# Optimization experiments

Measured on AMD Instinct MI355X. Metric: run time of the kernel, lower is better.

Reference implementation:

```python
import jax, jax.numpy as jnp
import numpy as np

NUM_HEADS = 8
CODEBOOK_SIZE = 1024
HEAD_DIM = 128
BATCH = 32768


def setup_inputs() -> dict:
    key = jax.random.key(0)
    k_z, k_cb = jax.random.split(key)
    z = jax.random.normal(k_z, (BATCH, NUM_HEADS * HEAD_DIM), dtype=jnp.float32)
    codebooks = jax.random.normal(k_cb, (NUM_HEADS, CODEBOOK_SIZE, HEAD_DIM), dtype=jnp.float32)
    return {"z": z, "codebooks": codebooks}


def reference(z, codebooks):
    # z: [B, H*D]; codebooks: [H, K, D]
    H, K, D = codebooks.shape
    B = z.shape[0]
    zh = z.reshape(B, H, D)
    # Squared euclidean distances ||z - c||^2 = ||z||^2 - 2 z.c + ||c||^2.
    # torch.cdist(p=2) applies sqrt, but sqrt is monotone so argmin is identical.
    z_sq = jnp.sum(zh * zh, axis=-1)                       # [B, H]
    c_sq = jnp.sum(codebooks * codebooks, axis=-1)         # [H, K]
    cross = jnp.einsum('bhd,hkd->bhk', zh, codebooks)      # [B, H, K]
    d2 = z_sq[:, :, None] - 2.0 * cross + c_sq[None, :, :]  # [B, H, K]
    idx = jnp.argmin(d2, axis=-1)                          # [B, H] int
    # Gather nearest codes per head: codebooks[h, idx[b,h]] -> [B, H, D]
    zq = codebooks[jnp.arange(H)[None, :], idx]
    # Straight-through estimator: forward = codes, backward = identity on z.
    zq = zh + jax.lax.stop_gradient(zq - zh)
    return zq.reshape(B, H * D), idx
```

## Files before the change

kernel.cpp:

```cpp
#include <hip/hip_runtime.h>

namespace {
constexpr int kNH = 8;
constexpr int kK  = 1024;
constexpr int kD  = 128;
constexpr int kB  = 32768;

constexpr int BM  = 128;
constexpr int kMarginQ = 4;
constexpr float kMarginF32 = 0.0625f;

constexpr size_t kOffCsq  = 4096;
constexpr size_t kOffCbF  = 65536;
constexpr size_t kOffPart = 65536 + 4194304;
constexpr size_t kOffWl6  = 65536 + 8388608;
constexpr size_t kOffWl5  = 65536 + 4194304;
}

typedef short           bf16x8 __attribute__((ext_vector_type(8)));
typedef unsigned short  us16x8 __attribute__((ext_vector_type(8)));
typedef float           f32x16 __attribute__((ext_vector_type(16)));

__device__ __forceinline__ unsigned short f2bf_rne(float f) {
    unsigned int x = __float_as_uint(f);
    unsigned int r = (x + 0x7fffu + ((x >> 16) & 1u)) >> 16;
    return (unsigned short)r;
}
__device__ __forceinline__ float bf2f(unsigned short u) {
    return __uint_as_float(((unsigned int)u) << 16);
}
__device__ __forceinline__ int med3_i32(int a, int b, int c) {
    int d;
    asm("v_med3_i32 %0, %1, %2, %3" : "=v"(d) : "v"(a), "v"(b), "v"(c));
    return d;
}

__global__ void pq_prep(const float* __restrict__ cb,
                        unsigned short* __restrict__ cbf,
                        float* __restrict__ csq)
{
    int code = blockIdx.x;
    int t = threadIdx.x;
    int h = code >> 10, k = code & 1023;
    int kt = k >> 6, cv = (k >> 5) & 1, l31 = k & 31;
    int kc = t >> 4, hh = (t >> 3) & 1, j = t & 7;
    float v = cb[(size_t)code * kD + t];
    float vs = v * -2048.0f;
    unsigned short hb = f2bf_rne(vs);
    unsigned short lb = f2bf_rne(vs - bf2f(hb));
    size_t base = ((((size_t)h * 16 + kt) * 8 + kc) * 2 + cv) * 2048;
    size_t off  = base + (hh * 32 + l31) * 16 + j * 2;
    *(unsigned short*)((char*)cbf + off)        = hb;
    *(unsigned short*)((char*)cbf + off + 1024) = lb;
    __shared__ double red[128];
    red[t] = (double)v * (double)v;
    __syncthreads();
    for (int s = 64; s > 0; s >>= 1) {
        if (t < s) red[t] += red[t + s];
        __syncthreads();
    }
    if (t == 0) csq[code] = (float)(red[0] * 1024.0);
}

__global__ __launch_bounds__(512)
void pq_coarse_mfma7(const float* __restrict__ z,
                     const unsigned short* __restrict__ cbf,
                     const float* __restrict__ csq1024,
                     int2* __restrict__ part)
{
    __shared__ unsigned short zbuf[2][2][32 * kD];
    __shared__ int2  P[2][8][32];
    __shared__ float csel_s[8][2][2][16];

    const int t    = threadIdx.x;
    const int lane = t & 63;
    const int w    = t >> 6;
    const int l31  = lane & 31, h32 = lane >> 5;
    const int h    = blockIdx.y;
    const int half = blockIdx.z;
    const int rb0  = blockIdx.x * 1024;

    {
        int ww = t >> 6, hb2 = (t >> 5) & 1, idx = t & 31;
        int cv = idx >> 4, r = idx & 15;
        int cr = (r & 3) + ((r >> 2) << 3);
        csel_s[ww][hb2][cv][r] =
            csq1024[h * kK + half * 512 + ww * 64 + hb2 * 4 + cv * 32 + cr];
    }

    const int cgb = half * 512 + w * 64 + h32 * 4;
    int addv[2][16];
    #pragma unroll
    for (int cv = 0; cv < 2; ++cv)
        #pragma unroll
        for (int r = 0; r < 16; ++r)
            addv[cv][r] = cgb + cv * 32 + (r & 3) + ((r >> 2) << 3);

    bf16x8 Ah[8][2], Al[8][2];
    {
        const char* base = (const char*)cbf
            + (((size_t)h * 16 + half * 8 + w) * 16) * 2048 + lane * 16;
        #pragma unroll
        for (int kc = 0; kc < 8; ++kc)
            #pragma unroll
            for (int cv = 0; cv < 2; ++cv) {
                const char* p = base + (size_t)(kc * 2 + cv) * 2048;
                Ah[kc][cv] = *(const bf16x8*)p;
                Al[kc][cv] = *(const bf16x8*)(p + 1024);
            }
    }

    float4 zA, zB;
    auto issueZ = [&](int tile) {
        const float* zp = z + (size_t)(rb0 + tile * 32 + (t >> 4)) * (kNH * kD)
                            + h * kD + (t & 15) * 8;
        zA = *(const float4*)zp;
        zB = *(const float4*)(zp + 4);
    };
    auto commitZ = [&](int buf) {
        unsigned u0 = __float_as_uint(zA.x) + 0x8000u;
        unsigned u1 = __float_as_uint(zA.y) + 0x8000u;
        unsigned u2 = __float_as_uint(zA.z) + 0x8000u;
        unsigned u3 = __float_as_uint(zA.w) + 0x8000u;
        unsigned u4 = __float_as_uint(zB.x) + 0x8000u;
        unsigned u5 = __float_as_uint(zB.y) + 0x8000u;
        unsigned u6 = __float_as_uint(zB.z) + 0x8000u;
        unsigned u7 = __float_as_uint(zB.w) + 0x8000u;
        unsigned h01 = __builtin_amdgcn_perm(u1, u0, 0x07060302u);
        unsigned h23 = __builtin_amdgcn_perm(u3, u2, 0x07060302u);
        unsigned h45 = __builtin_amdgcn_perm(u5, u4, 0x07060302u);
        unsigned h67 = __builtin_amdgcn_perm(u7, u6, 0x07060302u);
        float r0 = zA.x - __uint_as_float(u0 & 0xffff0000u);
        float r1 = zA.y - __uint_as_float(u1 & 0xffff0000u);
        float r2 = zA.z - __uint_as_float(u2 & 0xffff0000u);
        float r3 = zA.w - __uint_as_float(u3 & 0xffff0000u);
        float r4 = zB.x - __uint_as_float(u4 & 0xffff0000u);
        float r5 = zB.y - __uint_as_float(u5 & 0xffff0000u);
        float r6 = zB.z - __uint_as_float(u6 & 0xffff0000u);
        float r7 = zB.w - __uint_as_float(u7 & 0xffff0000u);
        unsigned l01 = __builtin_amdgcn_perm(__float_as_uint(r1) + 0x8000u,
                                             __float_as_uint(r0) + 0x8000u, 0x07060302u);
        unsigned l23 = __builtin_amdgcn_perm(__float_as_uint(r3) + 0x8000u,
                                             __float_as_uint(r2) + 0x8000u, 0x07060302u);
        unsigned l45 = __builtin_amdgcn_perm(__float_as_uint(r5) + 0x8000u,
                                             __float_as_uint(r4) + 0x8000u, 0x07060302u);
        unsigned l67 = __builtin_amdgcn_perm(__float_as_uint(r7) + 0x8000u,
                                             __float_as_uint(r6) + 0x8000u, 0x07060302u);
        int rr = t >> 4, seg = t & 15;
        int off = rr * 256 + ((seg * 16) ^ ((rr & 15) << 4));
        uint4 hv = {h01, h23, h45, h67};
        uint4 lv = {l01, l23, l45, l67};
        *(uint4*)((char*)&zbuf[buf][0][0] + off) = hv;
        *(uint4*)((char*)&zbuf[buf][1][0] + off) = lv;
    };
    auto mergeP = [&](int pb, int tile) {
        int2 m = P[pb][0][t];
        int m1 = m.x, m2 = m.y;
        #pragma unroll
        for (int ww = 1; ww < 8; ++ww) {
            int2 p = P[pb][ww][t];
            int mx = max(m1, p.x);
            m1 = min(m1, p.x);
            m2 = min(min(m2, p.y), mx);
        }
        int gid = (rb0 + tile * 32 + t) * kNH + h;
        part[(size_t)gid * 2 + half] = make_int2(m1, m2);
    };

    issueZ(0);
    commitZ(0);
    __syncthreads();

    int cur = 0;
    for (int tile = 0; tile < 32; ++tile) {
        if (tile + 1 < 32) issueZ(tile + 1);
        if (tile > 0 && t < 32) mergeP(cur ^ 1, tile - 1);

        f32x16 acc0, acc1;
        __builtin_memcpy(&acc0, &csel_s[w][h32][0][0], 64);
        __builtin_memcpy(&acc1, &csel_s[w][h32][1][0], 64);

        const char* zh0 = (const char*)&zbuf[cur][0][0];
        const char* zl0 = (const char*)&zbuf[cur][1][0];
        const int boff = l31 * 256;
        const int swz  = (l31 & 15) << 4;
        __builtin_amdgcn_s_setprio(1);
        #pragma unroll
        for (int kc = 0; kc < 8; ++kc) {
            int col = (kc * 32 + h32 * 16) ^ swz;
            bf16x8 Bh = *(const bf16x8*)(zh0 + boff + col);
            bf16x8 Bl = *(const bf16x8*)(zl0 + boff + col);
            acc0 = __builtin_amdgcn_mfma_f32_32x32x16_bf16(Ah[kc][0], Bh, acc0, 0, 0, 0);
            acc1 = __builtin_amdgcn_mfma_f32_32x32x16_bf16(Ah[kc][1], Bh, acc1, 0, 0, 0);
            acc0 = __builtin_amdgcn_mfma_f32_32x32x16_bf16(Al[kc][0], Bh, acc0, 0, 0, 0);
            acc1 = __builtin_amdgcn_mfma_f32_32x32x16_bf16(Al[kc][1], Bh, acc1, 0, 0, 0);
            acc0 = __builtin_amdgcn_mfma_f32_32x32x16_bf16(Ah[kc][0], Bl, acc0, 0, 0, 0);
            acc1 = __builtin_amdgcn_mfma_f32_32x32x16_bf16(Ah[kc][1], Bl, acc1, 0, 0, 0);
        }
        __builtin_amdgcn_s_setprio(0);

        if (tile + 1 < 32) commitZ(cur ^ 1);

        int b1 = 0x7fffffff, b2 = 0x7fffffff;
        #pragma unroll
        for (int r = 0; r < 16; ++r) {
            {
                int key = (((int)acc0[r]) << 10) + addv[0][r];
                b2 = med3_i32(key, b1, b2);
                b1 = min(b1, key);
            }
            {
                int key = (((int)acc1[r]) << 10) + addv[1][r];
                b2 = med3_i32(key, b1, b2);
                b1 = min(b1, key);
            }
        }
        int o1 = __shfl_xor(b1, 32), o2 = __shfl_xor(b2, 32);
        int mx2 = max(b1, o1);
        int v1 = min(b1, o1);
        int v2 = min(min(b2, o2), mx2);
        if (h32 == 0) P[cur][w][l31] = make_int2(v1, v2);

        __syncthreads();
        cur ^= 1;
    }
    if (t < 32) mergeP(cur ^ 1, 31);
}

__global__ __launch_bounds__(256)
void pq_merge(const int2* __restrict__ part, const float* __restrict__ cb,
              float* __restrict__ out_zq, float* __restrict__ out_idx,
              unsigned int* wl_count, unsigned int* wl, unsigned int wl_cap)
{
    __shared__ int idx_s[128];
    const int t = threadIdx.x;
    const int g0 = blockIdx.x * 128;
    if (t < 128) {
        int gid = g0 + t;
        int2 p0 = part[(size_t)gid * 2];
        int2 p1 = part[(size_t)gid * 2 + 1];
        int mx = max(p0.x, p1.x);
        int v1 = min(p0.x, p1.x);
        int v2 = min(min(p0.y, p1.y), mx);
        int idx = v1 & 1023;
        idx_s[t] = idx;
        out_idx[gid] = (float)idx;
        if (wl_cap > 0u && ((v2 >> 10) - (v1 >> 10)) <= kMarginQ) {
            unsigned int pos = atomicAdd(wl_count, 1u);
            if (pos < wl_cap) wl[pos] = (unsigned int)gid;
        }
    }
    __syncthreads();
    #pragma unroll
    for (int it = 0; it < 16; ++it) {
        int c = it * 256 + t;
        int row = c >> 5, c4 = c & 31;
        int gid = g0 + row;
        int b = gid >> 3, hh = gid & 7;
        *(float4*)(out_zq + (size_t)b * (kNH * kD) + hh * kD + c4 * 4) =
            *(const float4*)(cb + ((size_t)hh * kK + idx_s[row]) * kD + c4 * 4);
    }
}

__global__ __launch_bounds__(256, 2)
void pq_coarse_mfma3(const float* __restrict__ z, const float* __restrict__ cb,
                     const unsigned short* __restrict__ cbf,
                     const float* __restrict__ csq1024,
                     float* __restrict__ out_zq, float* __restrict__ out_idx,
                     unsigned int* wl_count, unsigned int* wl, unsigned int wl_cap)
{
    __shared__ float csq_s[kK];
    __shared__ int   idx_s[BM];

    const int t    = threadIdx.x;
    const int h    = blockIdx.y;
    const int b0   = blockIdx.x * BM;
    const int lane = t & 63;
    const int w    = t >> 6;
    const int l31  = lane & 31, h32 = lane >> 5;

    *(float4*)&csq_s[t * 4] = *(const float4*)(csq1024 + h * kK + t * 4);

    bf16x8 Ah[8], Al[8];
    {
        const float* zr = z + (size_t)(b0 + w * 32 + l31) * (kNH * kD) + h * kD + h32 * 8;
        #pragma unroll
        for (int kc = 0; kc < 8; ++kc) {
            float4 a = *(const float4*)(zr + kc * 16);
            float4 b = *(const float4*)(zr + kc * 16 + 4);
            float f[8] = {a.x, a.y, a.z, a.w, b.x, b.y, b.z, b.w};
            bf16x8 hv, lv;
            #pragma unroll
            for (int j = 0; j < 8; ++j) {
                unsigned short hb = f2bf_rne(f[j]);
                hv[j] = (short)hb;
                lv[j] = (short)f2bf_rne(f[j] - bf2f(hb));
            }
            Ah[kc] = hv;
            Al[kc] = lv;
        }
    }
    __syncthreads();

    int b1[16], b2[16];
    #pragma unroll
    for (int r = 0; r < 16; ++r) { b1[r] = 0x7fffffff; b2[r] = 0x7fffffff; }

    const char* bbase = (const char*)cbf + (size_t)h * 524288 + lane * 16;
#define LDSLOT(kt_, kc_, s_)                                                  \
    {                                                                         \
        const char* p_ = bbase + (size_t)(((kt_) * 8 + (kc_)) * 2) * 2048;    \
        Bh0[s_] = *(const bf16x8*)(p_);                                       \
        Bl0[s_] = *(const bf16x8*)(p_ + 1024);                                \
        Bh1[s_] = *(const bf16x8*)(p_ + 2048);                                \
        Bl1[s_] = *(const bf16x8*)(p_ + 3072);                                \
    }

    bf16x8 Bh0[4], Bl0[4], Bh1[4], Bl1[4];
    LDSLOT(0, 0, 0);
    LDSLOT(0, 1, 1);

    for (int kt = 0; kt < 16; ++kt) {
        f32x16 acc0 = (f32x16)0.0f, acc1 = (f32x16)0.0f;
        const int ktn = (kt + 1 < 16) ? kt + 1 : kt;
        #pragma unroll
        for (int kc = 0; kc < 8; ++kc) {
            const int s  = kc & 3;
            const int s2 = (kc + 2) & 3;
            if (kc < 6) { LDSLOT(kt, kc + 2, s2); } else { LDSLOT(ktn, kc - 6, s2); }
            __builtin_amdgcn_s_setprio(1);
            acc0 = __builtin_amdgcn_mfma_f32_32x32x16_bf16(Ah[kc], Bh0[s], acc0, 0, 0, 0);
            acc1 = __builtin_amdgcn_mfma_f32_32x32x16_bf16(Ah[kc], Bh1[s], acc1, 0, 0, 0);
            acc0 = __builtin_amdgcn_mfma_f32_32x32x16_bf16(Al[kc], Bh0[s], acc0, 0, 0, 0);
            acc1 = __builtin_amdgcn_mfma_f32_32x32x16_bf16(Al[kc], Bh1[s], acc1, 0, 0, 0);
            acc0 = __builtin_amdgcn_mfma_f32_32x32x16_bf16(Ah[kc], Bl0[s], acc0, 0, 0, 0);
            acc1 = __builtin_amdgcn_mfma_f32_32x32x16_bf16(Ah[kc], Bl1[s], acc1, 0, 0, 0);
            __builtin_amdgcn_s_setprio(0);
        }
        const float cs0 = csq_s[kt * 64 + l31];
        const float cs1 = csq_s[kt * 64 + 32 + l31];
        const int   kg0 = kt * 64 + l31, kg1 = kg0 + 32;
        #pragma unroll
        for (int r = 0; r < 16; ++r) {
            {
                float kf = acc0[r] + cs0;
                int key = ((int)kf << 10) + kg0;
                int mx = max(b1[r], key); b1[r] = min(b1[r], key); b2[r] = min(b2[r], mx);
            }
            {
                float kf = acc1[r] + cs1;
                int key = ((int)kf << 10) + kg1;
                int mx = max(b1[r], key); b1[r] = min(b1[r], key); b2[r] = min(b2[r], mx);
            }
        }
    }
#undef LDSLOT

    #pragma unroll
    for (int r = 0; r < 16; ++r) {
        int v1 = b1[r], v2 = b2[r];
        #pragma unroll
        for (int m = 1; m < 32; m <<= 1) {
            int o1 = __shfl_xor(v1, m);
            int o2 = __shfl_xor(v2, m);
            int mx = max(v1, o1);
            v1 = min(v1, o1);
            v2 = min(min(v2, o2), mx);
        }
        if (l31 == 0) {
            int row = w * 32 + (r & 3) + ((r >> 2) << 3) + h32 * 4;
            int idx = v1 & 1023;
            idx_s[row] = idx;
            int gid = (b0 + row) * kNH + h;
            out_idx[gid] = (float)idx;
            if (wl_cap > 0u && ((v2 >> 10) - (v1 >> 10)) <= kMarginQ) {
                unsigned int pos = atomicAdd(wl_count, 1u);
                if (pos < wl_cap) wl[pos] = (unsigned int)gid;
            }
        }
    }
    __syncthreads();
    {
        const float* cbh_row = cb + (size_t)h * kK * kD;
        #pragma unroll
        for (int it = 0; it < 16; ++it) {
            int c = it * 256 + t;
            int row = c >> 5, col4 = c & 31;
            *(float4*)(out_zq + (size_t)(b0 + row) * (kNH * kD) + h * kD + col4 * 4) =
                *(const float4*)(cbh_row + (size_t)idx_s[row] * kD + col4 * 4);
        }
    }
}

__global__ __launch_bounds__(256, 2)
void pq_coarse_f32(const float* __restrict__ z, const float* __restrict__ cb,
                   float* __restrict__ out_zq, float* __restrict__ out_idx,
                   unsigned int* wl_count, unsigned int* wl, unsigned int wl_cap)
{
    constexpr int KT = 64, PAD = 68, BMF = 64;
    __shared__ float zT[kD][PAD];
    __shared__ float cT[kD][PAD];
    __shared__ float csq_s[KT];
    __shared__ int   bidx_s[BMF];

    const int t  = threadIdx.x;
    const int h  = blockIdx.y;
    const int b0 = blockIdx.x * BMF;
    const int tx = t & 15, ty = t >> 4;
    const int r8 = t & 7,  d4 = t >> 3;

    {
        const float* zp = z + (size_t)(b0 + r8) * (kNH * kD) + h * kD + 4 * d4;
        #pragma unroll
        for (int it = 0; it < BMF / 8; ++it) {
            float4 v = *(const float4*)(zp + (size_t)(8 * it) * (kNH * kD));
            int r = r8 + 8 * it;
            zT[4 * d4 + 0][r] = v.x; zT[4 * d4 + 1][r] = v.y;
            zT[4 * d4 + 2][r] = v.z; zT[4 * d4 + 3][r] = v.w;
        }
    }
    float best1[4], best2[4]; int ibest[4];
    #pragma unroll
    for (int i = 0; i < 4; ++i) { best1[i] = 3.4e38f; best2[i] = 3.4e38f; ibest[i] = 0; }

    for (int kt = 0; kt < kK / KT; ++kt) {
        __syncthreads();
        {
            const float* cp = cb + ((size_t)h * kK + kt * KT + r8) * kD + 4 * d4;
            #pragma unroll
            for (int it = 0; it < KT / 8; ++it) {
                float4 v = *(const float4*)(cp + (size_t)(8 * it) * kD);
                int r = r8 + 8 * it;
                cT[4 * d4 + 0][r] = v.x; cT[4 * d4 + 1][r] = v.y;
                cT[4 * d4 + 2][r] = v.z; cT[4 * d4 + 3][r] = v.w;
            }
        }
        if (t < KT) csq_s[t] = 0.0f;
        __syncthreads();
        {
            int kk = t & 63, part = t >> 6;
            float s = 0.f;
            #pragma unroll
            for (int i = 0; i < 32; ++i) { float v = cT[32 * part + i][kk]; s = fmaf(v, v, s); }
            atomicAdd(&csq_s[kk], s);
        }
        __syncthreads();
        float accA[4][4] = {{0}}, accB[4][4] = {{0}};
        #pragma unroll 2
        for (int d = 0; d < kD; d += 2) {
            float4 za = *(const float4*)&zT[d][4 * ty];
            float4 ca = *(const float4*)&cT[d][4 * tx];
            float4 zb = *(const float4*)&zT[d + 1][4 * ty];
            float4 cv = *(const float4*)&cT[d + 1][4 * tx];
            float zav[4] = {za.x, za.y, za.z, za.w}, cav[4] = {ca.x, ca.y, ca.z, ca.w};
            float zbv[4] = {zb.x, zb.y, zb.z, zb.w}, cbv[4] = {cv.x, cv.y, cv.z, cv.w};
            #pragma unroll
            for (int i = 0; i < 4; ++i)
                #pragma unroll
                for (int j = 0; j < 4; ++j) {
                    accA[i][j] = fmaf(zav[i], cav[j], accA[i][j]);
                    accB[i][j] = fmaf(zbv[i], cbv[j], accB[i][j]);
                }
        }
        #pragma unroll
        for (int j = 0; j < 4; ++j) {
            int kk = 4 * tx + j;
            float cs = csq_s[kk];
            int kg = kt * KT + kk;
            #pragma unroll
            for (int i = 0; i < 4; ++i) {
                float s = fmaf(-2.0f, accA[i][j] + accB[i][j], cs);
                if (s < best1[i]) { best2[i] = best1[i]; best1[i] = s; ibest[i] = kg; }
                else if (s < best2[i]) { best2[i] = s; }
            }
        }
    }
    __syncthreads();
    float* redv1 = &zT[0][0];
    float* redv2 = redv1 + BMF * 16;
    int*   redi  = (int*)(redv2 + BMF * 16);
    #pragma unroll
    for (int i = 0; i < 4; ++i) {
        int r = 4 * ty + i;
        redv1[r * 16 + tx] = best1[i]; redv2[r * 16 + tx] = best2[i]; redi[r * 16 + tx] = ibest[i];
    }
    __syncthreads();
    if (t < BMF) {
        int r = t;
        float vb1_ = redv1[r * 16], vb2_ = redv2[r * 16];
        int i1 = redi[r * 16];
        #pragma unroll
        for (int x = 1; x < 16; ++x) {
            float nb1 = redv1[r * 16 + x], nb2 = redv2[r * 16 + x];
            int ni1 = redi[r * 16 + x];
            if (nb1 < vb1_ || (nb1 == vb1_ && ni1 < i1)) { vb2_ = fminf(vb1_, nb2); vb1_ = nb1; i1 = ni1; }
            else vb2_ = fminf(vb2_, nb1);
        }
        bidx_s[r] = i1;
        int gid = (b0 + r) * kNH + h;
        out_idx[gid] = (float)i1;
        if (wl_cap > 0u && (vb2_ - vb1_) <= kMarginF32) {
            unsigned int pos = atomicAdd(wl_count, 1u);
            if (pos < wl_cap) wl[pos] = (unsigned int)gid;
        }
    }
    __syncthreads();
    {
        int r = t >> 2, q = t & 3;
        const float* src = cb + ((size_t)h * kK + bidx_s[r]) * kD;
        float* dst = out_zq + (size_t)(b0 + r) * (kNH * kD) + h * kD;
        #pragma unroll
        for (int m = 0; m < 8; ++m) {
            int jj = 4 * m + q;
            *(float4*)(dst + 4 * jj) = *(const float4*)(src + 4 * jj);
        }
    }
}

__global__ __launch_bounds__(256)
void pq_exact(const float* __restrict__ z, const float* __restrict__ cb,
              float* __restrict__ out_zq, float* __restrict__ out_idx,
              const unsigned int* wl_count, const unsigned int* wl,
              unsigned int wl_cap)
{
    if (wl_cap == 0u) return;
    __shared__ float  zs[kD];
    __shared__ double rv[256];
    __shared__ int    ri[256];
    unsigned int n = *wl_count;
    if (n > wl_cap) n = wl_cap;
    const int t = threadIdx.x;
    for (unsigned int e = blockIdx.x; e < n; e += gridDim.x) {
        unsigned int id = wl[e];
        int b = (int)(id / kNH), h = (int)(id % kNH);
        if (t < kD) zs[t] = z[(size_t)b * (kNH * kD) + h * kD + t];
        __syncthreads();
        double bv = 1e300; int bi = 0;
        #pragma unroll
        for (int kk = 0; kk < 4; ++kk) {
            int k = t * 4 + kk;
            const float* c = cb + ((size_t)h * kK + k) * kD;
            double s = 0.0;
            for (int d = 0; d < kD; ++d) {
                double diff = (double)zs[d] - (double)c[d];
                s = fma(diff, diff, s);
            }
            if (s < bv) { bv = s; bi = k; }
        }
        rv[t] = bv; ri[t] = bi;
        __syncthreads();
        for (int s2 = 128; s2 > 0; s2 >>= 1) {
            if (t < s2) {
                if (rv[t + s2] < rv[t] || (rv[t + s2] == rv[t] && ri[t + s2] < ri[t])) {
                    rv[t] = rv[t + s2]; ri[t] = ri[t + s2];
                }
            }
            __syncthreads();
        }
        int kbest = ri[0];
        if (t == 0) out_idx[id] = (float)kbest;
        if (t < kD)
            out_zq[(size_t)b * (kNH * kD) + h * kD + t] =
                cb[((size_t)h * kK + kbest) * kD + t];
        __syncthreads();
    }
}

extern "C" void kernel_launch(void* const* d_in, const int* in_sizes, int n_in,
                              void* d_out, int out_size, void* d_ws, size_t ws_size,
                              hipStream_t stream)
{
    const float* z  = (const float*)d_in[0];
    const float* cb = (const float*)d_in[1];
    float* out_zq  = (float*)d_out;
    float* out_idx = out_zq + (size_t)kB * kNH * kD;
    char* ws = (char*)d_ws;

    if (ws_size >= kOffWl6 + 65536) {
        unsigned int* wl_count = (unsigned int*)ws;
        unsigned int* wl = (unsigned int*)(ws + kOffWl6);
        size_t c = (ws_size - kOffWl6) / 4;
        unsigned int cap = (unsigned int)(c > 262144 ? 262144 : c);
        float* csq = (float*)(ws + kOffCsq);
        unsigned short* cbf = (unsigned short*)(ws + kOffCbF);
        int2* part = (int2*)(ws + kOffPart);

        hipMemsetAsync(d_ws, 0, 4, stream);
        pq_prep<<<kNH * kK, kD, 0, stream>>>(cb, cbf, csq);
        dim3 grid(32, kNH, 2);
        pq_coarse_mfma7<<<grid, 512, 0, stream>>>(z, cbf, csq, part);
        pq_merge<<<kB * kNH / 128, 256, 0, stream>>>(part, cb, out_zq, out_idx,
                                                     wl_count, wl, cap);
        pq_exact<<<256, 256, 0, stream>>>(z, cb, out_zq, out_idx, wl_count, wl, cap);
    } else if (ws_size >= kOffWl5 + 4096) {
        unsigned int* wl_count = (unsigned int*)ws;
        unsigned int* wl = (unsigned int*)(ws + kOffWl5);
        size_t c = (ws_size - kOffWl5) / 4;
        unsigned int cap = (unsigned int)(c > 262144 ? 262144 : c);
        float* csq = (float*)(ws + kOffCsq);
        unsigned short* cbf = (unsigned short*)(ws + kOffCbF);

        hipMemsetAsync(d_ws, 0, 4, stream);
        pq_prep<<<kNH * kK, kD, 0, stream>>>(cb, cbf, csq);
        dim3 grid(kB / BM, kNH);
        pq_coarse_mfma3<<<grid, 256, 0, stream>>>(z, cb, cbf, csq,
                                                  out_zq, out_idx, wl_count, wl, cap);
        pq_exact<<<256, 256, 0, stream>>>(z, cb, out_zq, out_idx, wl_count, wl, cap);
    } else {
        unsigned int* wl_count = (unsigned int*)ws;
        unsigned int* wl = wl_count + 1;
        unsigned int cap = 0;
        if (ws_size >= 64) {
            size_t c = ws_size / 4 - 1;
            cap = (unsigned int)(c > 262144 ? 262144 : c);
            hipMemsetAsync(d_ws, 0, 4, stream);
        }
        dim3 grid(kB / 64, kNH);
        pq_coarse_f32<<<grid, 256, 0, stream>>>(z, cb, out_zq, out_idx, wl_count, wl, cap);
        pq_exact<<<256, 256, 0, stream>>>(z, cb, out_zq, out_idx, wl_count, wl, cap);
    }
}
```

Baseline: 226.4 us.

## Cover full codebook per block with 1024 threads, drop two-half partial merge

The coarse MFMA kernel now uses 16 waves per block so one block scans all 1024 codes for its rows instead of splitting the codebook into two halves across blocks. This halves redundant z loads and conversion, halves the partial-result buffer, and removes the two-way merge in pq_merge. In exchange the grid has half as many blocks, each with 1024 threads, which may lower occupancy and latency hiding and lengthens the intra-block merge.

```diff
diff --git a/kernel.cpp b/kernel.cpp
--- a/kernel.cpp
+++ b/kernel.cpp
@@ -13,12 +13,11 @@
 constexpr size_t kOffCsq  = 4096;
 constexpr size_t kOffCbF  = 65536;
 constexpr size_t kOffPart = 65536 + 4194304;
-constexpr size_t kOffWl6  = 65536 + 8388608;
+constexpr size_t kOffWl10 = 65536 + 4194304 + 2097152;
 constexpr size_t kOffWl5  = 65536 + 4194304;
 }
 
 typedef short           bf16x8 __attribute__((ext_vector_type(8)));
-typedef unsigned short  us16x8 __attribute__((ext_vector_type(8)));
 typedef float           f32x16 __attribute__((ext_vector_type(16)));
 
 __device__ __forceinline__ unsigned short f2bf_rne(float f) {
@@ -62,22 +61,21 @@
     if (t == 0) csq[code] = (float)(red[0] * 1024.0);
 }
 
-__global__ __launch_bounds__(512)
-void pq_coarse_mfma7(const float* __restrict__ z,
-                     const unsigned short* __restrict__ cbf,
-                     const float* __restrict__ csq1024,
-                     int2* __restrict__ part)
+__global__ __launch_bounds__(1024)
+void pq_coarse_mfma10(const float* __restrict__ z,
+                      const unsigned short* __restrict__ cbf,
+                      const float* __restrict__ csq1024,
+                      int2* __restrict__ part)
 {
     __shared__ unsigned short zbuf[2][2][32 * kD];
-    __shared__ int2  P[2][8][32];
-    __shared__ float csel_s[8][2][2][16];
+    __shared__ int2  P[2][16][32];
+    __shared__ float csel_s[16][2][2][16];
 
     const int t    = threadIdx.x;
     const int lane = t & 63;
     const int w    = t >> 6;
     const int l31  = lane & 31, h32 = lane >> 5;
     const int h    = blockIdx.y;
-    const int half = blockIdx.z;
     const int rb0  = blockIdx.x * 1024;
 
     {
@@ -85,10 +83,10 @@
         int cv = idx >> 4, r = idx & 15;
         int cr = (r & 3) + ((r >> 2) << 3);
         csel_s[ww][hb2][cv][r] =
-            csq1024[h * kK + half * 512 + ww * 64 + hb2 * 4 + cv * 32 + cr];
-    }
-
-    const int cgb = half * 512 + w * 64 + h32 * 4;
+            csq1024[h * kK + ww * 64 + hb2 * 4 + cv * 32 + cr];
+    }
+
+    const int cgb = w * 64 + h32 * 4;
     int addv[2][16];
     #pragma unroll
     for (int cv = 0; cv < 2; ++cv)
@@ -99,7 +97,7 @@
     bf16x8 Ah[8][2], Al[8][2];
     {
         const char* base = (const char*)cbf
-            + (((size_t)h * 16 + half * 8 + w) * 16) * 2048 + lane * 16;
+            + (((size_t)h * 16 + w) * 16) * 2048 + lane * 16;
         #pragma unroll
         for (int kc = 0; kc < 8; ++kc)
             #pragma unroll
@@ -110,61 +108,44 @@
             }
     }
 
-    float4 zA, zB;
+    float4 zA;
     auto issueZ = [&](int tile) {
-        const float* zp = z + (size_t)(rb0 + tile * 32 + (t >> 4)) * (kNH * kD)
-                            + h * kD + (t & 15) * 8;
-        zA = *(const float4*)zp;
-        zB = *(const float4*)(zp + 4);
+        zA = *(const float4*)(z + (size_t)(rb0 + tile * 32 + (t >> 5)) * (kNH * kD)
+                                + h * kD + (t & 31) * 4);
     };
     auto commitZ = [&](int buf) {
         unsigned u0 = __float_as_uint(zA.x) + 0x8000u;
         unsigned u1 = __float_as_uint(zA.y) + 0x8000u;
         unsigned u2 = __float_as_uint(zA.z) + 0x8000u;
         unsigned u3 = __float_as_uint(zA.w) + 0x8000u;
-        unsigned u4 = __float_as_uint(zB.x) + 0x8000u;
-        unsigned u5 = __float_as_uint(zB.y) + 0x8000u;
-        unsigned u6 = __float_as_uint(zB.z) + 0x8000u;
-        unsigned u7 = __float_as_uint(zB.w) + 0x8000u;
         unsigned h01 = __builtin_amdgcn_perm(u1, u0, 0x07060302u);
         unsigned h23 = __builtin_amdgcn_perm(u3, u2, 0x07060302u);
-        unsigned h45 = __builtin_amdgcn_perm(u5, u4, 0x07060302u);
-        unsigned h67 = __builtin_amdgcn_perm(u7, u6, 0x07060302u);
         float r0 = zA.x - __uint_as_float(u0 & 0xffff0000u);
         float r1 = zA.y - __uint_as_float(u1 & 0xffff0000u);
         float r2 = zA.z - __uint_as_float(u2 & 0xffff0000u);
         float r3 = zA.w - __uint_as_float(u3 & 0xffff0000u);
-        float r4 = zB.x - __uint_as_float(u4 & 0xffff0000u);
-        float r5 = zB.y - __uint_as_float(u5 & 0xffff0000u);
-        float r6 = zB.z - __uint_as_float(u6 & 0xffff0000u);
-        float r7 = zB.w - __uint_as_float(u7 & 0xffff0000u);
         unsigned l01 = __builtin_amdgcn_perm(__float_as_uint(r1) + 0x8000u,
                                              __float_as_uint(r0) + 0x8000u, 0x07060302u);
         unsigned l23 = __builtin_amdgcn_perm(__float_as_uint(r3) + 0x8000u,
                                              __float_as_uint(r2) + 0x8000u, 0x07060302u);
-        unsigned l45 = __builtin_amdgcn_perm(__float_as_uint(r5) + 0x8000u,
-                                             __float_as_uint(r4) + 0x8000u, 0x07060302u);
-        unsigned l67 = __builtin_amdgcn_perm(__float_as_uint(r7) + 0x8000u,
-                                             __float_as_uint(r6) + 0x8000u, 0x07060302u);
-        int rr = t >> 4, seg = t & 15;
-        int off = rr * 256 + ((seg * 16) ^ ((rr & 15) << 4));
-        uint4 hv = {h01, h23, h45, h67};
-        uint4 lv = {l01, l23, l45, l67};
-        *(uint4*)((char*)&zbuf[buf][0][0] + off) = hv;
-        *(uint4*)((char*)&zbuf[buf][1][0] + off) = lv;
+        int rr = t >> 5, c4 = t & 31;
+        int off = rr * 256 + ((((c4 >> 1) * 16)) ^ ((rr & 15) << 4)) + (c4 & 1) * 8;
+        uint2 hv = {h01, h23};
+        uint2 lv = {l01, l23};
+        *(uint2*)((char*)&zbuf[buf][0][0] + off) = hv;
+        *(uint2*)((char*)&zbuf[buf][1][0] + off) = lv;
     };
     auto mergeP = [&](int pb, int tile) {
         int2 m = P[pb][0][t];
         int m1 = m.x, m2 = m.y;
         #pragma unroll
-        for (int ww = 1; ww < 8; ++ww) {
+        for (int ww = 1; ww < 16; ++ww) {
             int2 p = P[pb][ww][t];
             int mx = max(m1, p.x);
             m1 = min(m1, p.x);
             m2 = min(min(m2, p.y), mx);
         }
-        int gid = (rb0 + tile * 32 + t) * kNH + h;
-        part[(size_t)gid * 2 + half] = make_int2(m1, m2);
+        part[(size_t)(rb0 + tile * 32 + t) * kNH + h] = make_int2(m1, m2);
     };
 
     issueZ(0);
@@ -237,15 +218,11 @@
     const int g0 = blockIdx.x * 128;
     if (t < 128) {
         int gid = g0 + t;
-        int2 p0 = part[(size_t)gid * 2];
-        int2 p1 = part[(size_t)gid * 2 + 1];
-        int mx = max(p0.x, p1.x);
-        int v1 = min(p0.x, p1.x);
-        int v2 = min(min(p0.y, p1.y), mx);
-        int idx = v1 & 1023;
+        int2 p = part[gid];
+        int idx = p.x & 1023;
         idx_s[t] = idx;
         out_idx[gid] = (float)idx;
-        if (wl_cap > 0u && ((v2 >> 10) - (v1 >> 10)) <= kMarginQ) {
+        if (wl_cap > 0u && ((p.y >> 10) - (p.x >> 10)) <= kMarginQ) {
             unsigned int pos = atomicAdd(wl_count, 1u);
             if (pos < wl_cap) wl[pos] = (unsigned int)gid;
         }
@@ -576,10 +553,10 @@
     float* out_idx = out_zq + (size_t)kB * kNH * kD;
     char* ws = (char*)d_ws;
 
-    if (ws_size >= kOffWl6 + 65536) {
+    if (ws_size >= kOffWl10 + 65536) {
         unsigned int* wl_count = (unsigned int*)ws;
-        unsigned int* wl = (unsigned int*)(ws + kOffWl6);
-        size_t c = (ws_size - kOffWl6) / 4;
+        unsigned int* wl = (unsigned int*)(ws + kOffWl10);
+        size_t c = (ws_size - kOffWl10) / 4;
         unsigned int cap = (unsigned int)(c > 262144 ? 262144 : c);
         float* csq = (float*)(ws + kOffCsq);
         unsigned short* cbf = (unsigned short*)(ws + kOffCbF);
@@ -587,8 +564,8 @@
 
         hipMemsetAsync(d_ws, 0, 4, stream);
         pq_prep<<<kNH * kK, kD, 0, stream>>>(cb, cbf, csq);
-        dim3 grid(32, kNH, 2);
-        pq_coarse_mfma7<<<grid, 512, 0, stream>>>(z, cbf, csq, part);
+        dim3 grid(32, kNH);
+        pq_coarse_mfma10<<<grid, 1024, 0, stream>>>(z, cbf, csq, part);
         pq_merge<<<kB * kNH / 128, 256, 0, stream>>>(part, cb, out_zq, out_idx,
                                                      wl_count, wl, cap);
         pq_exact<<<256, 256, 0, stream>>>(z, cb, out_zq, out_idx, wl_count, wl, cap);
```

New measurement: 471.2 us. 2.08x slower.
